# Kernel optimization log

Hardware: AMD Instinct MI355X
Metric: run time of the kernel (lower is better)

The kernel has to match this reference:

```python
import jax, jax.numpy as jnp
import numpy as np

V, E, H, K, B, T = 50000, 256, 512, 12, 32, 256
START, STOP = 10, 11
NEG = -10000.0
Hd = H // 2


def _lstm(x, h0, c0, Wih, Whh, bih, bhh):
    # x: [T, B, D] -> hidden states [T, B, Hd]; PyTorch gate order i,f,g,o
    def step(carry, xt):
        h, c = carry
        g = xt @ Wih.T + bih + h @ Whh.T + bhh
        i, f, gg, o = jnp.split(g, 4, axis=-1)
        c = jax.nn.sigmoid(f) * c + jax.nn.sigmoid(i) * jnp.tanh(gg)
        h = jax.nn.sigmoid(o) * jnp.tanh(c)
        return (h, c), h
    _, hs = jax.lax.scan(step, (h0, c0), x)
    return hs


def setup_inputs() -> dict:
    key = jax.random.key(0)
    ks = jax.random.split(key, 12)
    inp = {}
    inp["sentence"] = jax.random.randint(ks[0], (B, T), 0, V, dtype=jnp.int32)
    lens = jax.random.randint(ks[1], (B,), 1, T + 1, dtype=jnp.int32)
    inp["seq_lens"] = jnp.sort(lens)[::-1]  # pack_padded requires descending
    emb = jax.random.normal(ks[2], (V, E)) * 0.05
    inp["emb"] = emb.at[0].set(0.0)  # padding_idx=0
    def lw(k):
        a, b, c, d = jax.random.split(k, 4)
        return (jax.random.normal(a, (4 * Hd, E)) * 0.05,
                jax.random.normal(b, (4 * Hd, Hd)) * 0.05,
                jax.random.normal(c, (4 * Hd,)) * 0.05,
                jax.random.normal(d, (4 * Hd,)) * 0.05)
    inp["Wih_f"], inp["Whh_f"], inp["bih_f"], inp["bhh_f"] = lw(ks[3])
    inp["Wih_b"], inp["Whh_b"], inp["bih_b"], inp["bhh_b"] = lw(ks[4])
    inp["h0"] = jax.random.normal(ks[5], (2, B, Hd))  # init_hidden uses randn
    inp["c0"] = jax.random.normal(ks[6], (2, B, Hd))
    inp["W_out"] = jax.random.normal(ks[7], (K, H)) * 0.05
    inp["b_out"] = jax.random.normal(ks[8], (K,)) * 0.05
    trans = jax.random.normal(ks[9], (K, K))
    inp["transitions"] = trans.at[START, :].set(NEG).at[:, STOP].set(NEG)
    return inp


def _features(sentence, seq_lens, emb, Wih_f, Whh_f, bih_f, bhh_f,
              Wih_b, Whh_b, bih_b, bhh_b, h0, c0, W_out, b_out):
    x = emb[sentence]                       # [B,T,E]
    t_idx = jnp.arange(T)
    # forward direction
    hf = _lstm(x.transpose(1, 0, 2), h0[0], c0[0], Wih_f, Whh_f, bih_f, bhh_f)
    hf = hf.transpose(1, 0, 2)              # [B,T,Hd]
    # backward direction: reverse each sequence within its length (packed semantics)
    rev_idx = jnp.where(t_idx[None, :] < seq_lens[:, None],
                        seq_lens[:, None] - 1 - t_idx[None, :], t_idx[None, :])  # [B,T]
    x_rev = jnp.take_along_axis(x, rev_idx[:, :, None], axis=1)
    hb_rev = _lstm(x_rev.transpose(1, 0, 2), h0[1], c0[1], Wih_b, Whh_b, bih_b, bhh_b)
    hb = jnp.take_along_axis(hb_rev.transpose(1, 0, 2), rev_idx[:, :, None], axis=1)
    hcat = jnp.concatenate([hf, hb], axis=-1)  # [B,T,H]
    return hcat @ W_out.T + b_out              # [B,T,K]


def _viterbi(feats, seq_lens, transitions):
    t_idx = jnp.arange(T)
    mask = t_idx[None, :] < seq_lens[:, None]           # [B,T]
    init = jnp.full((B, K), NEG).at[:, START].set(0.0)  # forward_var

    def vstep(fv, inputs):
        feat_t, m_t = inputs                            # [B,K], [B]
        scores = fv[:, None, :] + transitions[None, :, :]   # [B, next, prev]
        bp = jnp.argmax(scores, axis=-1)                # [B,K]
        best = jnp.max(scores, axis=-1) + feat_t
        return jnp.where(m_t[:, None], best, fv), bp

    fv, bps = jax.lax.scan(vstep, init, (feats.transpose(1, 0, 2), mask.T))
    terminal = fv + transitions[STOP][None, :]          # [B,K]
    best_last = jnp.argmax(terminal, axis=-1)           # [B]
    path_scores = jnp.take_along_axis(terminal, best_last[:, None], axis=1)[:, 0]

    def btstep(tag, inputs):
        bp_t, m_t = inputs
        pred_t = jnp.where(m_t, tag, -1)
        prev = jnp.take_along_axis(bp_t, tag[:, None], axis=1)[:, 0]
        return jnp.where(m_t, prev, tag), pred_t

    _, preds_rev = jax.lax.scan(btstep, best_last, (bps[::-1], mask.T[::-1]))
    preds = preds_rev[::-1].transpose(1, 0)             # [B,T], -1 past seq_len
    return path_scores, preds


def reference(sentence, seq_lens, emb, Wih_f, Whh_f, bih_f, bhh_f,
              Wih_b, Whh_b, bih_b, bhh_b, h0, c0, W_out, b_out, transitions):
    feats = _features(sentence, seq_lens, emb, Wih_f, Whh_f, bih_f, bhh_f,
                      Wih_b, Whh_b, bih_b, bhh_b, h0, c0, W_out, b_out)
    scores, preds = _viterbi(feats, seq_lens, transitions)
    return scores, preds
```

## Files before the change

kernel.cpp:

```cpp
#include <hip/hip_runtime.h>
#include <math.h>

#define T_ 256
#define B_ 32
#define E_ 256
#define HD_ 256
#define NG_ 1024
#define K_ 12
#define START_ 10
#define STOP_ 11
#define NEG_ -10000.0f
#define MAGICU 0x40000000u

typedef float f4_t __attribute__((ext_vector_type(4)));

__device__ __forceinline__ float sigf(float x) { return 1.0f / (1.0f + expf(-x)); }

__global__ void prep(const int* __restrict__ sent, const int* __restrict__ lens,
                     int* __restrict__ tokA, const float* __restrict__ Wf,
                     const float* __restrict__ Wb, float* __restrict__ WT,
                     float* __restrict__ hex, int* __restrict__ gcnt) {
    const int b = blockIdx.x, tid = threadIdx.x;
    if (b < 4096) {
        float4 m = make_float4(2.0f, 2.0f, 2.0f, 2.0f);
        ((float4*)hex)[b * 256 + tid] = m;
        if (b == 0 && tid < 128) gcnt[tid] = 0;
    } else if (b < 4608) {
        int b2 = b - 4096;
        int dir = b2 >> 8, k = b2 & 255, u = tid;
        const float* W = dir ? Wb : Wf;
        float4 v;
        v.x = W[(0 * HD_ + u) * HD_ + k];
        v.y = W[(1 * HD_ + u) * HD_ + k];
        v.z = W[(2 * HD_ + u) * HD_ + k];
        v.w = W[(3 * HD_ + u) * HD_ + k];
        ((float4*)(WT + ((size_t)dir * 256 + k) * NG_))[u] = v;
    } else {
        int e = (b - 4608) * 256 + tid;
        int dir = e >> 13, m = e & 8191, t = m >> 5, bb = m & 31;
        int len = lens[bb];
        int tt = dir ? (t < len ? len - 1 - t : t) : t;
        tokA[e] = sent[bb * T_ + tt];
    }
}

__global__ __launch_bounds__(512, 1) void mega(
    const float* __restrict__ emb, const int* __restrict__ tokA,
    const float* __restrict__ Wih_f, const float* __restrict__ Wih_b,
    const float* __restrict__ bih_f, const float* __restrict__ bhh_f,
    const float* __restrict__ bih_b, const float* __restrict__ bhh_b,
    const float* __restrict__ WhhT, float* __restrict__ G,
    const float* __restrict__ h0, const float* __restrict__ c0,
    const int* __restrict__ lens, float* __restrict__ hex,
    int* __restrict__ gcnt, const float* __restrict__ Wout,
    const float* __restrict__ bout, float* __restrict__ feats) {
    __shared__ float smem[24832];
    const int tid = threadIdx.x;

    if (blockIdx.x >= 1088) {
        const int blk = blockIdx.x - 1088;
        f4_t* hbuf = (f4_t*)smem;
#pragma unroll
        for (int i = 0; i < 8; ++i) {
            int idx = i * 512 + tid;
            int pl = idx >> 7, j = idx & 127;
            int p = blk * 32 + pl;
            int b = p >> 8, t = p & 255;
            int len = lens[b];
            int g = b >> 3;
            int Tg = lens[g * 8];
            const float* addr;
            if (j < 64) {
                addr = hex + ((size_t)g * T_ + t) * 2048 + (b & 7) * 256 + j * 4;
            } else {
                int tr = t < len ? len - 1 - t : t;
                addr = hex + ((size_t)(4 + g) * T_ + tr) * 2048 + (b & 7) * 256 + (j - 64) * 4;
            }
            float a0 = __hip_atomic_load(addr + 0, __ATOMIC_RELAXED, __HIP_MEMORY_SCOPE_AGENT);
            float a1 = __hip_atomic_load(addr + 1, __ATOMIC_RELAXED, __HIP_MEMORY_SCOPE_AGENT);
            float a2 = __hip_atomic_load(addr + 2, __ATOMIC_RELAXED, __HIP_MEMORY_SCOPE_AGENT);
            float a3 = __hip_atomic_load(addr + 3, __ATOMIC_RELAXED, __HIP_MEMORY_SCOPE_AGENT);
            if (t < Tg) {
                int it = 0;
                while (__float_as_uint(a0) == MAGICU || __float_as_uint(a1) == MAGICU ||
                       __float_as_uint(a2) == MAGICU || __float_as_uint(a3) == MAGICU) {
                    __builtin_amdgcn_s_sleep(2);
                    a0 = __hip_atomic_load(addr + 0, __ATOMIC_RELAXED, __HIP_MEMORY_SCOPE_AGENT);
                    a1 = __hip_atomic_load(addr + 1, __ATOMIC_RELAXED, __HIP_MEMORY_SCOPE_AGENT);
                    a2 = __hip_atomic_load(addr + 2, __ATOMIC_RELAXED, __HIP_MEMORY_SCOPE_AGENT);
                    a3 = __hip_atomic_load(addr + 3, __ATOMIC_RELAXED, __HIP_MEMORY_SCOPE_AGENT);
                    if (++it > (1 << 22)) break;
                }
            }
            f4_t v; v.x = a0; v.y = a1; v.z = a2; v.w = a3;
            hbuf[pl * 129 + j] = v;
        }
        __syncthreads();
        if (tid < 384) {
            int pl = tid / 12, k = tid - pl * 12;
            int p = blk * 32 + pl;
            const float4* w0 = (const float4*)(Wout + (size_t)k * 512);
            const f4_t* hrow = hbuf + pl * 129;
            float acc = bout[k];
#pragma unroll 4
            for (int j = 0; j < 128; ++j) {
                f4_t h4 = hrow[j];
                float4 v4 = w0[j];
                acc += h4.x * v4.x + h4.y * v4.y + h4.z * v4.z + h4.w * v4.w;
            }
            feats[(size_t)p * K_ + k] = acc;
        }
        return;
    }

    if (blockIdx.x >= 64) {
        const int bi = blockIdx.x - 64;
        const int by = bi >> 4, sub = bi & 15;
        const int dir = sub >> 3, bx = sub & 7;
        const int n0 = bx * 128, m0 = by * 128;
        float* As = smem;
        float* Bs = smem + 1024;
        const int rs = (tid & 255) >> 1, kc = (tid & 1) * 4;
        const float* srow;
        if (tid < 256) {
            int tok = tokA[dir * 8192 + m0 + rs];
            srow = emb + (size_t)tok * E_;
        } else {
            int np = n0 + rs;
            int wrow = ((np & 3) << 8) | (np >> 2);
            srow = (dir ? Wih_b : Wih_f) + (size_t)wrow * E_;
        }
        float* Ls = (tid < 256) ? As : Bs;
        const int ty = tid >> 4, tx = tid & 15;

        float acc[4][8];
#pragma unroll
        for (int i = 0; i < 4; ++i)
#pragma unroll
            for (int j = 0; j < 8; ++j) acc[i][j] = 0.f;

        for (int k0 = 0; k0 < E_; k0 += 8) {
            float4 v = *(const float4*)(srow + k0 + kc);
            __syncthreads();
            Ls[(kc + 0) * 128 + rs] = v.x;
            Ls[(kc + 1) * 128 + rs] = v.y;
            Ls[(kc + 2) * 128 + rs] = v.z;
            Ls[(kc + 3) * 128 + rs] = v.w;
            __syncthreads();
#pragma unroll
            for (int k = 0; k < 8; ++k) {
                float4 a  = *(const float4*)&As[k * 128 + ty * 4];
                float4 b0 = *(const float4*)&Bs[k * 128 + tx * 8];
                float4 b1 = *(const float4*)&Bs[k * 128 + tx * 8 + 4];
                float af[4] = {a.x, a.y, a.z, a.w};
                float bf[8] = {b0.x, b0.y, b0.z, b0.w, b1.x, b1.y, b1.z, b1.w};
#pragma unroll
                for (int i = 0; i < 4; ++i)
#pragma unroll
                    for (int j = 0; j < 8; ++j) acc[i][j] += af[i] * bf[j];
            }
        }
        const float* bihp = dir ? bih_b : bih_f;
        const float* bhhp = dir ? bhh_b : bhh_f;
        float bias[8];
#pragma unroll
        for (int j = 0; j < 8; ++j) {
            int nn = n0 + tx * 8 + j;
            int wr = ((nn & 3) << 8) | (nn >> 2);
            bias[j] = bihp[wr] + bhhp[wr];
        }
#pragma unroll
        for (int i = 0; i < 4; ++i) {
            int m = m0 + ty * 4 + i;
            float* gp = G + ((size_t)dir * 8192 + m) * NG_ + n0 + tx * 8;
            f4_t o0, o1;
            o0.x = acc[i][0] + bias[0]; o0.y = acc[i][1] + bias[1];
            o0.z = acc[i][2] + bias[2]; o0.w = acc[i][3] + bias[3];
            o1.x = acc[i][4] + bias[4]; o1.y = acc[i][5] + bias[5];
            o1.z = acc[i][6] + bias[6]; o1.w = acc[i][7] + bias[7];
            asm volatile("global_store_dwordx4 %0, %1, off sc0 sc1" :: "v"(gp), "v"(o0) : "memory");
            asm volatile("global_store_dwordx4 %0, %1, off sc0 sc1" :: "v"(gp + 4), "v"(o1) : "memory");
        }
        asm volatile("s_waitcnt vmcnt(0)" ::: "memory");
        __syncthreads();
        if (tid == 0)
            __hip_atomic_fetch_add(gcnt + dir * 64 + by, 1,
                                   __ATOMIC_RELEASE, __HIP_MEMORY_SCOPE_AGENT);
        return;
    }

    float4* red4 = (float4*)smem;
    float4* hsA4 = (float4*)(smem + 22528);
    float4* hsB4 = (float4*)(smem + 23552);
    float4* hT4  = (float4*)(smem + 24576);

    const int wg = blockIdx.x;
    const int dir = wg >> 5, bt = (wg >> 3) & 3, ut = wg & 7;
    const int wv = tid >> 6, ln = tid & 63;
    const int upair = ln & 15;
    const int kssub = ln >> 4;
    const int ksup = wv >> 1, bh = wv & 1;
    const int ks = ksup * 4 + kssub;
    const int sb = bh * 4 + (ln & 3);
    const int sk = ksup * 64 + (ln >> 2) * 4;
    const int speer = sk >> 5;

    const int Tmax = lens[bt * 8];

    const float4* WT4 = (const float4*)(WhhT + (size_t)dir * 256 * NG_);
    const int gu_e = ut * 32 + upair * 2;
    float4 We[16], Wo[16];
#pragma unroll
    for (int j = 0; j < 16; ++j) {
        We[j] = WT4[(ks * 16 + j) * 256 + gu_e];
        Wo[j] = WT4[(ks * 16 + j) * 256 + gu_e + 1];
    }

    {
        int it = 0;
        while (__hip_atomic_load(gcnt + dir * 64, __ATOMIC_RELAXED, __HIP_MEMORY_SCOPE_AGENT) < 8) {
            __builtin_amdgcn_s_sleep(8);
            if (++it > (1 << 22)) break;
        }
    }

    const bool is_act = (ln < 32);
    float c = 0.f;
    float4 gpend = make_float4(0.f, 0.f, 0.f, 0.f);
    const float* Gd = G + (size_t)dir * 8192 * NG_;
    int gok = 1, gready = 0;
    if (is_act) {
        c = c0[(dir * B_ + bt * 8 + wv) * HD_ + ut * 32 + ln];
        gpend = ((const float4*)(Gd + (size_t)(bt * 8 + wv) * NG_))[ut * 32 + ln];
    }

    float* hexg = hex + (size_t)(dir * 4 + bt) * T_ * 2048;
    float4* hsX4 = bh ? hsB4 : hsA4;
    float* hsX = (float*)hsX4;

    f4_t pend;

    for (int t = 0; t < Tmax; ++t) {
        float4 hv;
        if (t == 0) {
            hv = *(const float4*)(h0 + (size_t)(dir * B_ + bt * 8 + sb) * HD_ + sk);
        } else if (speer == ut) {
            hv = hT4[sb * 8 + ((sk & 31) >> 2)];
        } else {
            asm volatile("s_waitcnt vmcnt(0)" ::: "memory");
            hv.x = pend.x; hv.y = pend.y; hv.z = pend.z; hv.w = pend.w;
            if (__float_as_uint(hv.x) == MAGICU || __float_as_uint(hv.y) == MAGICU ||
                __float_as_uint(hv.z) == MAGICU || __float_as_uint(hv.w) == MAGICU) {
                const float* src = hexg + (size_t)(t - 1) * 2048 + sb * 256 + sk;
                int it = 0;
                for (;;) {
                    __builtin_amdgcn_s_sleep(1);
                    float a0 = __hip_atomic_load(src + 0, __ATOMIC_RELAXED, __HIP_MEMORY_SCOPE_AGENT);
                    float a1 = __hip_atomic_load(src + 1, __ATOMIC_RELAXED, __HIP_MEMORY_SCOPE_AGENT);
                    float a2 = __hip_atomic_load(src + 2, __ATOMIC_RELAXED, __HIP_MEMORY_SCOPE_AGENT);
                    float a3 = __hip_atomic_load(src + 3, __ATOMIC_RELAXED, __HIP_MEMORY_SCOPE_AGENT);
                    if (!(__float_as_uint(a0) == MAGICU || __float_as_uint(a1) == MAGICU ||
                          __float_as_uint(a2) == MAGICU || __float_as_uint(a3) == MAGICU)) {
                        hv = make_float4(a0, a1, a2, a3); break;
                    }
                    if (++it > (1 << 22)) break;
                }
            }
        }
        hsX[(sk + 0) * 4 + (ln & 3)] = hv.x;
        hsX[(sk + 1) * 4 + (ln & 3)] = hv.y;
        hsX[(sk + 2) * 4 + (ln & 3)] = hv.z;
        hsX[(sk + 3) * 4 + (ln & 3)] = hv.w;
        asm volatile("s_waitcnt lgkmcnt(0)" ::: "memory");

        float4 ae0 = {0,0,0,0}, ae1 = {0,0,0,0}, ae2 = {0,0,0,0}, ae3 = {0,0,0,0};
        float4 ao0 = {0,0,0,0}, ao1 = {0,0,0,0}, ao2 = {0,0,0,0}, ao3 = {0,0,0,0};
#pragma unroll
        for (int j = 0; j < 16; ++j) {
            float4 h4 = hsX4[ks * 16 + j];
            float4 we = We[j], wo = Wo[j];
            ae0.x += we.x*h4.x; ae0.y += we.y*h4.x; ae0.z += we.z*h4.x; ae0.w += we.w*h4.x;
            ae1.x += we.x*h4.y; ae1.y += we.y*h4.y; ae1.z += we.z*h4.y; ae1.w += we.w*h4.y;
            ae2.x += we.x*h4.z; ae2.y += we.y*h4.z; ae2.z += we.z*h4.z; ae2.w += we.w*h4.z;
            ae3.x += we.x*h4.w; ae3.y += we.y*h4.w; ae3.z += we.z*h4.w; ae3.w += we.w*h4.w;
            ao0.x += wo.x*h4.x; ao0.y += wo.y*h4.x; ao0.z += wo.z*h4.x; ao0.w += wo.w*h4.x;
            ao1.x += wo.x*h4.y; ao1.y += wo.y*h4.y; ao1.z += wo.z*h4.y; ao1.w += wo.w*h4.y;
            ao2.x += wo.x*h4.z; ao2.y += wo.y*h4.z; ao2.z += wo.z*h4.z; ao2.w += wo.w*h4.z;
            ao3.x += wo.x*h4.w; ao3.y += wo.y*h4.w; ao3.z += wo.z*h4.w; ao3.w += wo.w*h4.w;
        }
        {
            float4* r = &red4[((wv * 4 + kssub) * 16 + upair) * 11 + kssub];
            r[0] = ae0; r[1] = ae1; r[2] = ae2; r[3] = ae3;
            r[4] = ao0; r[5] = ao1; r[6] = ao2; r[7] = ao3;
        }
        asm volatile("s_waitcnt lgkmcnt(0)\n\ts_barrier" ::: "memory");

        if (is_act) {
            const int b = wv, u = ln;
            const int bhv = b >> 2, bq = b & 3, up = u >> 1, par = u & 1;
            if (!gok) {
                const int byc = t >> 2;
                int itc = 0;
                while (__hip_atomic_load(gcnt + dir * 64 + byc, __ATOMIC_RELAXED,
                                         __HIP_MEMORY_SCOPE_AGENT) < 8) {
                    __builtin_amdgcn_s_sleep(2);
                    if (++itc > (1 << 22)) break;
                }
                const float* gsrc = Gd + ((size_t)t * B_ + bt * 8 + b) * NG_ + (size_t)(ut * 32 + u) * 4;
                f4_t tmp;
                asm volatile("global_load_dwordx4 %0, %1, off sc0 sc1\n\ts_waitcnt vmcnt(0)"
                             : "=v"(tmp) : "v"(gsrc) : "memory");
                gpend = make_float4(tmp.x, tmp.y, tmp.z, tmp.w);
            }
            float si = gpend.x, sf = gpend.y, sg = gpend.z, so = gpend.w;
#pragma unroll
            for (int kq = 0; kq < 4; ++kq)
#pragma unroll
                for (int kr = 0; kr < 4; ++kr) {
                    float4 p = red4[(((kq * 2 + bhv) * 4 + kr) * 16 + up) * 11 + kr + par * 4 + bq];
                    si += p.x; sf += p.y; sg += p.z; so += p.w;
                }
            c = sigf(sf) * c + sigf(si) * tanhf(sg);
            float h = sigf(so) * tanhf(c);
            ((float*)hT4)[b * 32 + u] = h;
            float* dst = hexg + (size_t)t * 2048 + b * 256 + ut * 32 + u;
            asm volatile("global_store_dword %0, %1, off sc0 sc1" :: "v"(dst), "v"(h) : "memory");
            if (t + 1 < Tmax) {
                const int byn = (t + 1) >> 2;
                if (byn > gready) {
                    int la = byn + 7; if (la > 63) la = 63;
                    if (__hip_atomic_load(gcnt + dir * 64 + la, __ATOMIC_RELAXED,
                                          __HIP_MEMORY_SCOPE_AGENT) >= 8) gready = la;
                    else if (__hip_atomic_load(gcnt + dir * 64 + byn, __ATOMIC_RELAXED,
                                               __HIP_MEMORY_SCOPE_AGENT) >= 8) gready = byn;
                }
                if (byn <= gready) {
                    gpend = ((const float4*)(Gd + ((size_t)(t + 1) * B_ + bt * 8 + b) * NG_))[ut * 32 + u];
                    gok = 1;
                } else gok = 0;
            }
        }
        if (t + 1 < Tmax && speer != ut) {
            const float* nsrc = hexg + (size_t)t * 2048 + sb * 256 + sk;
            asm volatile("global_load_dwordx4 %0, %1, off sc0 sc1"
                         : "=v"(pend) : "v"(nsrc) : "memory");
        }
        asm volatile("s_waitcnt lgkmcnt(0)\n\ts_barrier" ::: "memory");
    }
}

__global__ __launch_bounds__(512) void viterbi_k(
    const float* __restrict__ feats, const float* __restrict__ trans,
    const int* __restrict__ lens, float* __restrict__ out) {
    __shared__ float fv[2][B_][16];
    __shared__ float tl[K_][16];
    __shared__ unsigned char bp[T_][B_][6];
    __shared__ int best_last[B_];
    int tid = threadIdx.x;
    int b = tid >> 4, lane = tid & 15;
    if (tid < K_ * K_) tl[tid / 12][tid % 12] = trans[tid];
    if (lane < K_) fv[0][b][lane] = (lane == START_) ? 0.f : NEG_;
    __syncthreads();
    int len = lens[b];
    int pp = 0;
    float f_cur = 0.f;
    if (lane < K_) f_cur = feats[(size_t)b * T_ * K_ + lane];
    for (int t = 0; t < T_; ++t) {
        float f_nxt = 0.f;
        if (t + 1 < T_ && lane < K_) f_nxt = feats[((size_t)b * T_ + t + 1) * K_ + lane];
        if (lane < K_) {
            float best = fv[pp][b][0] + tl[lane][0];
            int argp = 0;
#pragma unroll
            for (int p = 1; p < K_; ++p) {
                float v = fv[pp][b][p] + tl[lane][p];
                if (v > best) { best = v; argp = p; }
            }
            float nb = best + f_cur;
            fv[pp ^ 1][b][lane] = (t < len) ? nb : fv[pp][b][lane];
            int other = __shfl_xor(argp, 1);
            if ((lane & 1) == 0) bp[t][b][lane >> 1] = (unsigned char)(argp | (other << 4));
        }
        __syncthreads();
        pp ^= 1;
        f_cur = f_nxt;
    }
    if (lane == 0) {
        float best = fv[pp][b][0] + tl[STOP_][0];
        int bl = 0;
#pragma unroll
        for (int p = 1; p < K_; ++p) {
            float v = fv[pp][b][p] + tl[STOP_][p];
            if (v > best) { best = v; bl = p; }
        }
        out[b] = best;
        best_last[b] = bl;
    }
    __syncthreads();
    if (lane == 0) {
        int tag = best_last[b];
        for (int t = T_ - 1; t >= 0; --t) {
            int m = (t < len);
            out[B_ + b * T_ + t] = (float)(m ? tag : -1);
            if (m) tag = (bp[t][b][tag >> 1] >> ((tag & 1) * 4)) & 15;
        }
    }
}

extern "C" void kernel_launch(void* const* d_in, const int* in_sizes, int n_in,
                              void* d_out, int out_size, void* d_ws, size_t ws_size,
                              hipStream_t stream) {
    const int*   sent  = (const int*)d_in[0];
    const int*   lens  = (const int*)d_in[1];
    const float* emb   = (const float*)d_in[2];
    const float* Wih_f = (const float*)d_in[3];
    const float* Whh_f = (const float*)d_in[4];
    const float* bih_f = (const float*)d_in[5];
    const float* bhh_f = (const float*)d_in[6];
    const float* Wih_b = (const float*)d_in[7];
    const float* Whh_b = (const float*)d_in[8];
    const float* bih_b = (const float*)d_in[9];
    const float* bhh_b = (const float*)d_in[10];
    const float* h0    = (const float*)d_in[11];
    const float* c0    = (const float*)d_in[12];
    const float* Wout  = (const float*)d_in[13];
    const float* bout  = (const float*)d_in[14];
    const float* trans = (const float*)d_in[15];
    float* out = (float*)d_out;

    char* ws = (char*)d_ws;
    int*   tokA  = (int*)ws;
    float* WhhT  = (float*)(ws + 65536);
    float* G     = (float*)(ws + 2162688);
    float* feats = (float*)(ws + 69271552);
    float* hex   = (float*)(ws + 69664768);
    int*   gcnt  = (int*)(out + 32);

    prep<<<4672, 256, 0, stream>>>(sent, lens, tokA, Whh_f, Whh_b, WhhT, hex, gcnt);
    mega<<<1344, 512, 0, stream>>>(emb, tokA, Wih_f, Wih_b, bih_f, bhh_f, bih_b, bhh_b,
                                   WhhT, G, h0, c0, lens, hex, gcnt, Wout, bout, feats);
    viterbi_k<<<1, 512, 0, stream>>>(feats, trans, lens, out);
}
```

Baseline: 1.103 ms.

## Fuse Viterbi into mega kernel as a block consuming feature chunks via flags

```diff
diff --git a/kernel.cpp b/kernel.cpp
--- a/kernel.cpp
+++ b/kernel.cpp
@@ -24,7 +24,7 @@
     if (b < 4096) {
         float4 m = make_float4(2.0f, 2.0f, 2.0f, 2.0f);
         ((float4*)hex)[b * 256 + tid] = m;
-        if (b == 0 && tid < 128) gcnt[tid] = 0;
+        if (b == 0 && tid < 136) gcnt[tid] = 0;
     } else if (b < 4608) {
         int b2 = b - 4096;
         int dir = b2 >> 8, k = b2 & 255, u = tid;
@@ -53,9 +53,95 @@
     const float* __restrict__ h0, const float* __restrict__ c0,
     const int* __restrict__ lens, float* __restrict__ hex,
     int* __restrict__ gcnt, const float* __restrict__ Wout,
-    const float* __restrict__ bout, float* __restrict__ feats) {
+    const float* __restrict__ bout, float* __restrict__ feats,
+    const float* __restrict__ trans, float* __restrict__ out) {
     __shared__ float smem[24832];
     const int tid = threadIdx.x;
+
+    if (blockIdx.x == 1344) {
+        unsigned char* bp = (unsigned char*)smem;
+        float* fv = smem + 12288;
+        float* tl = smem + 13312;
+        int* best_last = (int*)(smem + 13504);
+        float* fbuf = smem + 13536;
+        int* fcnt = gcnt + 128;
+        const int b = tid >> 4, lane = tid & 15;
+        if (tid < K_ * K_) tl[(tid / 12) * 16 + (tid % 12)] = trans[tid];
+        if (lane < K_) fv[b * 16 + lane] = (lane == START_) ? 0.f : NEG_;
+        __syncthreads();
+        const int len = lens[b];
+        int pp = 0;
+        for (int tc = 0; tc < 16; ++tc) {
+            if (tid == 0) {
+                int it = 0;
+                while (__hip_atomic_load(fcnt + (tc >> 1), __ATOMIC_RELAXED,
+                                         __HIP_MEMORY_SCOPE_AGENT) < 32) {
+                    __builtin_amdgcn_s_sleep(16);
+                    if (++it > (1 << 22)) break;
+                }
+            }
+            __syncthreads();
+            {
+                const int bb = tid >> 4, dt = tid & 15;
+                const int t = tc * 16 + dt;
+                const float* src = feats + (size_t)(bb * 256 + t) * K_;
+                f4_t v0, v1, v2;
+                asm volatile("global_load_dwordx4 %0, %3, off sc0 sc1\n\t"
+                             "global_load_dwordx4 %1, %4, off sc0 sc1\n\t"
+                             "global_load_dwordx4 %2, %5, off sc0 sc1\n\t"
+                             "s_waitcnt vmcnt(0)"
+                             : "=v"(v0), "=v"(v1), "=v"(v2)
+                             : "v"(src), "v"(src + 4), "v"(src + 8) : "memory");
+                float* d = fbuf + (dt * 32 + bb) * 13;
+                d[0] = v0.x; d[1] = v0.y; d[2]  = v0.z; d[3]  = v0.w;
+                d[4] = v1.x; d[5] = v1.y; d[6]  = v1.z; d[7]  = v1.w;
+                d[8] = v2.x; d[9] = v2.y; d[10] = v2.z; d[11] = v2.w;
+            }
+            __syncthreads();
+            for (int dt = 0; dt < 16; ++dt) {
+                const int t = tc * 16 + dt;
+                if (lane < K_) {
+                    float f_cur = fbuf[(dt * 32 + b) * 13 + lane];
+                    float best = fv[pp * 512 + b * 16 + 0] + tl[lane * 16 + 0];
+                    int argp = 0;
+#pragma unroll
+                    for (int p = 1; p < K_; ++p) {
+                        float v = fv[pp * 512 + b * 16 + p] + tl[lane * 16 + p];
+                        if (v > best) { best = v; argp = p; }
+                    }
+                    float nb = best + f_cur;
+                    fv[(pp ^ 1) * 512 + b * 16 + lane] =
+                        (t < len) ? nb : fv[pp * 512 + b * 16 + lane];
+                    int other = __shfl_xor(argp, 1);
+                    if ((lane & 1) == 0)
+                        bp[(t * 32 + b) * 6 + (lane >> 1)] = (unsigned char)(argp | (other << 4));
+                }
+                __syncthreads();
+                pp ^= 1;
+            }
+        }
+        if (lane == 0) {
+            float best = fv[pp * 512 + b * 16 + 0] + tl[STOP_ * 16 + 0];
+            int bl = 0;
+#pragma unroll
+            for (int p = 1; p < K_; ++p) {
+                float v = fv[pp * 512 + b * 16 + p] + tl[STOP_ * 16 + p];
+                if (v > best) { best = v; bl = p; }
+            }
+            out[b] = best;
+            best_last[b] = bl;
+        }
+        __syncthreads();
+        if (lane == 0) {
+            int tag = best_last[b];
+            for (int t = T_ - 1; t >= 0; --t) {
+                int m = (t < len);
+                out[B_ + b * T_ + t] = (float)(m ? tag : -1);
+                if (m) tag = (bp[(t * 32 + b) * 6 + (tag >> 1)] >> ((tag & 1) * 4)) & 15;
+            }
+        }
+        return;
+    }
 
     if (blockIdx.x >= 1088) {
         const int blk = blockIdx.x - 1088;
@@ -108,8 +194,14 @@
                 float4 v4 = w0[j];
                 acc += h4.x * v4.x + h4.y * v4.y + h4.z * v4.z + h4.w * v4.w;
             }
-            feats[(size_t)p * K_ + k] = acc;
-        }
+            float* fdst = feats + (size_t)p * K_ + k;
+            asm volatile("global_store_dword %0, %1, off sc0 sc1" :: "v"(fdst), "v"(acc) : "memory");
+        }
+        asm volatile("s_waitcnt vmcnt(0)" ::: "memory");
+        __syncthreads();
+        if (tid == 0)
+            __hip_atomic_fetch_add(gcnt + 128 + (blk & 7), 1,
+                                   __ATOMIC_RELEASE, __HIP_MEMORY_SCOPE_AGENT);
         return;
     }
 
@@ -349,64 +441,6 @@
     }
 }
 
-__global__ __launch_bounds__(512) void viterbi_k(
-    const float* __restrict__ feats, const float* __restrict__ trans,
-    const int* __restrict__ lens, float* __restrict__ out) {
-    __shared__ float fv[2][B_][16];
-    __shared__ float tl[K_][16];
-    __shared__ unsigned char bp[T_][B_][6];
-    __shared__ int best_last[B_];
-    int tid = threadIdx.x;
-    int b = tid >> 4, lane = tid & 15;
-    if (tid < K_ * K_) tl[tid / 12][tid % 12] = trans[tid];
-    if (lane < K_) fv[0][b][lane] = (lane == START_) ? 0.f : NEG_;
-    __syncthreads();
-    int len = lens[b];
-    int pp = 0;
-    float f_cur = 0.f;
-    if (lane < K_) f_cur = feats[(size_t)b * T_ * K_ + lane];
-    for (int t = 0; t < T_; ++t) {
-        float f_nxt = 0.f;
-        if (t + 1 < T_ && lane < K_) f_nxt = feats[((size_t)b * T_ + t + 1) * K_ + lane];
-        if (lane < K_) {
-            float best = fv[pp][b][0] + tl[lane][0];
-            int argp = 0;
-#pragma unroll
-            for (int p = 1; p < K_; ++p) {
-                float v = fv[pp][b][p] + tl[lane][p];
-                if (v > best) { best = v; argp = p; }
-            }
-            float nb = best + f_cur;
-            fv[pp ^ 1][b][lane] = (t < len) ? nb : fv[pp][b][lane];
-            int other = __shfl_xor(argp, 1);
-            if ((lane & 1) == 0) bp[t][b][lane >> 1] = (unsigned char)(argp | (other << 4));
-        }
-        __syncthreads();
-        pp ^= 1;
-        f_cur = f_nxt;
-    }
-    if (lane == 0) {
-        float best = fv[pp][b][0] + tl[STOP_][0];
-        int bl = 0;
-#pragma unroll
-        for (int p = 1; p < K_; ++p) {
-            float v = fv[pp][b][p] + tl[STOP_][p];
-            if (v > best) { best = v; bl = p; }
-        }
-        out[b] = best;
-        best_last[b] = bl;
-    }
-    __syncthreads();
-    if (lane == 0) {
-        int tag = best_last[b];
-        for (int t = T_ - 1; t >= 0; --t) {
-            int m = (t < len);
-            out[B_ + b * T_ + t] = (float)(m ? tag : -1);
-            if (m) tag = (bp[t][b][tag >> 1] >> ((tag & 1) * 4)) & 15;
-        }
-    }
-}
-
 extern "C" void kernel_launch(void* const* d_in, const int* in_sizes, int n_in,
                               void* d_out, int out_size, void* d_ws, size_t ws_size,
                               hipStream_t stream) {
@@ -437,7 +471,7 @@
     int*   gcnt  = (int*)(out + 32);
 
     prep<<<4672, 256, 0, stream>>>(sent, lens, tokA, Whh_f, Whh_b, WhhT, hex, gcnt);
-    mega<<<1344, 512, 0, stream>>>(emb, tokA, Wih_f, Wih_b, bih_f, bhh_f, bih_b, bhh_b,
-                                   WhhT, G, h0, c0, lens, hex, gcnt, Wout, bout, feats);
-    viterbi_k<<<1, 512, 0, stream>>>(feats, trans, lens, out);
+    mega<<<1345, 512, 0, stream>>>(emb, tokA, Wih_f, Wih_b, bih_f, bhh_f, bih_b, bhh_b,
+                                   WhhT, G, h0, c0, lens, hex, gcnt, Wout, bout, feats,
+                                   trans, out);
 }
```

Measured after the change: 1.193 ms. +8.1%, slower.
